# Optimization experiments

Hardware: AMD Instinct MI355X
Metric: run time of the kernel (lower is better)

## Reference

```python
import jax, jax.numpy as jnp
import numpy as np

D = 128          # hidden_channels
NU = 50000       # num user nodes
NI = 50000       # num item nodes
E = 600000       # edges per edge type
SLOPE = 0.01     # F.leaky_relu default negative_slope


def setup_inputs() -> dict:
    key = jax.random.key(0)
    ks = jax.random.split(key, 24)
    ws = 1.0 / np.sqrt(D)  # xavier-ish scale

    def W2(i):  # stacked [n_layers=2, D, D] weight
        return jax.random.normal(ks[i], (2, D, D), jnp.float32) * ws

    def B2(i):  # stacked [2, D] bias
        return jax.random.normal(ks[i], (2, D), jnp.float32) * 0.01

    inp = {
        "x_user": jax.random.normal(ks[0], (NU, D), jnp.float32),
        "x_item": jax.random.normal(ks[1], (NI, D), jnp.float32),
        # row 0 = src indices, row 1 = dst indices
        "ei_ui": jax.random.randint(ks[2], (2, E), 0, NU),  # user -> item (dst in [0,NI))
        "ei_iu": jax.random.randint(ks[3], (2, E), 0, NI),  # item -> user (dst in [0,NU))
        # per-node-type q/k/v Linear params, stacked over the 2 layers
        "q_w_user": W2(4),  "q_b_user": B2(5),
        "k_w_user": W2(6),  "k_b_user": B2(7),
        "v_w_user": W2(8),  "v_b_user": B2(9),
        "q_w_item": W2(10), "q_b_item": B2(11),
        "k_w_item": W2(12), "k_b_item": B2(13),
        "v_w_item": W2(14), "v_b_item": B2(15),
        # per-edge-type bilinear W, stacked over the 2 layers
        "W_ui": W2(16),
        "W_iu": W2(17),
    }
    return inp


def _edge_agg(x_src, x_dst, qw, qb, kw, kb, vw, vb, W, src, dst, n_dst):
    # torch Linear: x @ w.T + b
    q = x_src @ qw.T + qb            # [Nsrc, D]
    k = x_dst @ kw.T + kb            # [Ndst, D]
    v = x_src @ vw.T + vb            # [Nsrc, D]
    qW = q @ W                       # project on nodes (cheaper than per-edge)
    # per-edge bilinear score q_src . W . k_dst / sqrt(D)
    score = jnp.sum(qW[src] * k[dst], axis=-1) * (1.0 / np.sqrt(D))  # [E]
    alpha = jax.nn.softmax(jax.nn.leaky_relu(score, SLOPE))          # softmax over edges
    msg = alpha[:, None] * v[src]                                    # [E, D]
    return jax.ops.segment_sum(msg, dst, num_segments=n_dst)


def _layer(x_u, x_i, ei_ui, ei_iu, p, l):
    # edge type (user, rates, item): q/v from src type (user), k from dst type (item)
    agg_i = _edge_agg(x_u, x_i,
                      p["q_w_user"][l], p["q_b_user"][l],
                      p["k_w_item"][l], p["k_b_item"][l],
                      p["v_w_user"][l], p["v_b_user"][l],
                      p["W_ui"][l], ei_ui[0], ei_ui[1], NI)
    # edge type (item, rev_rates, user)
    agg_u = _edge_agg(x_i, x_u,
                      p["q_w_item"][l], p["q_b_item"][l],
                      p["k_w_user"][l], p["k_b_user"][l],
                      p["v_w_item"][l], p["v_b_item"][l],
                      p["W_iu"][l], ei_iu[0], ei_iu[1], NU)
    # out_dict initialized with x_dst.clone(), then scatter_add
    return x_u + agg_u, x_i + agg_i


def reference(x_user, x_item, ei_ui, ei_iu,
              q_w_user, q_b_user, k_w_user, k_b_user, v_w_user, v_b_user,
              q_w_item, q_b_item, k_w_item, k_b_item, v_w_item, v_b_item,
              W_ui, W_iu):
    p = dict(q_w_user=q_w_user, q_b_user=q_b_user, k_w_user=k_w_user,
             k_b_user=k_b_user, v_w_user=v_w_user, v_b_user=v_b_user,
             q_w_item=q_w_item, q_b_item=q_b_item, k_w_item=k_w_item,
             k_b_item=k_b_item, v_w_item=v_w_item, v_b_item=v_b_item,
             W_ui=W_ui, W_iu=W_iu)
    x_u, x_i = _layer(x_user, x_item, ei_ui, ei_iu, p, 0)  # conv1
    x_u, x_i = _layer(x_u, x_i, ei_ui, ei_iu, p, 1)        # conv2
    return jnp.concatenate([x_u, x_i], axis=0)  # [NU+NI, D]
```

## Files before the change

### kernel.cpp

```cpp
#include <hip/hip_runtime.h>
#include <stdint.h>

#define D 128

typedef __attribute__((ext_vector_type(8))) short bf16x8;
typedef __attribute__((ext_vector_type(4))) float f32x4;
typedef __attribute__((ext_vector_type(2))) float f32x2;
typedef unsigned short u16;
typedef unsigned char u8;
typedef unsigned int u32;

#define KSCALE (0.08838834764831845f * 1.4426950408889634f)

static __device__ __forceinline__ float b2f(u16 u) {
  return __uint_as_float(((unsigned)u) << 16);
}
static __device__ __forceinline__ u16 f2b(float f) {
  unsigned u = __float_as_uint(f);
  return (u16)((u + 0x7fffu + ((u >> 16) & 1u)) >> 16);
}

#if defined(__has_builtin)
#if __has_builtin(__builtin_amdgcn_cvt_pk_f32_fp8) && __has_builtin(__builtin_amdgcn_cvt_pk_fp8_f32)
#define HW_FP8 1
#endif
#endif

static __device__ __forceinline__ u8 enc_fp8(float f) {
#ifdef HW_FP8
  int p = __builtin_amdgcn_cvt_pk_fp8_f32(f, 0.f, 0, false);
  return (u8)(p & 0xff);
#else
  float a = fabsf(f);
  unsigned s = (__float_as_uint(f) >> 31) << 7;
  if (a < 7.8125e-3f) {
    int m = (int)(a * 512.f + 0.5f);
    if (m > 7) m = 7;
    return (u8)(s | m);
  }
  int e; float mant = frexpf(a, &e);
  int E = e + 6;
  int m = (int)((2.f * mant - 1.f) * 8.f + 0.5f);
  if (m == 8) { m = 0; E++; }
  if (E > 15 || (E == 15 && m > 6)) { E = 15; m = 6; }
  if (E < 1) return (u8)s;
  return (u8)(s | (E << 3) | m);
#endif
}

static __device__ __forceinline__ float dec1_fp8(u8 b) {
  int e = (b >> 3) & 15, m = b & 7;
  float mag = e ? ldexpf((float)(8 + m), e - 10) : ldexpf((float)m, -9);
  return (b & 128) ? -mag : mag;
}

static __device__ __forceinline__ void dec8_fp8(u32 lo, u32 hi, float* o) {
#ifdef HW_FP8
  f32x2 a = __builtin_amdgcn_cvt_pk_f32_fp8((int)lo, false);
  f32x2 b = __builtin_amdgcn_cvt_pk_f32_fp8((int)lo, true);
  f32x2 c = __builtin_amdgcn_cvt_pk_f32_fp8((int)hi, false);
  f32x2 d = __builtin_amdgcn_cvt_pk_f32_fp8((int)hi, true);
  o[0] = a.x; o[1] = a.y; o[2] = b.x; o[3] = b.y;
  o[4] = c.x; o[5] = c.y; o[6] = d.x; o[7] = d.y;
#else
  u32 w[2] = {lo, hi};
  u8* p = (u8*)w;
#pragma unroll
  for (int i = 0; i < 8; ++i) o[i] = dec1_fp8(p[i]);
#endif
}

template <int CTRL>
static __device__ __forceinline__ float dpp_add_f(float x) {
  int y = __builtin_amdgcn_update_dpp(0, __float_as_int(x), CTRL, 0xf, 0xf, true);
  return x + __int_as_float(y);
}

__global__ void prep_fused(const float* __restrict__ qwu, const float* __restrict__ qbu,
                           const float* __restrict__ qwi, const float* __restrict__ qbi,
                           const float* __restrict__ Wui, const float* __restrict__ Wiu,
                           u16* __restrict__ Mt, float* __restrict__ bq) {
  int c = blockIdx.y, d = blockIdx.x, j = threadIdx.x;
  int l = c & 1, type = c >> 1;
  const float* qw = (type ? qwi : qwu) + l * D * D;
  const float* qb = (type ? qbi : qbu) + l * D;
  const float* W  = (type ? Wiu : Wui) + l * D * D;
  float acc = 0.f;
  for (int cc = 0; cc < D; ++cc) acc += qw[cc * D + d] * W[cc * D + j];
  Mt[((size_t)c * D + j) * D + d] = f2b(acc);
  if (d == 0) {
    float ba = 0.f;
    for (int cc = 0; cc < D; ++cc) ba += qb[cc] * W[cc * D + j];
    bq[c * D + j] = ba;
  }
}

__global__ void cast_w(const float* __restrict__ kwu, const float* __restrict__ kwi,
                       const float* __restrict__ vwu, const float* __restrict__ vwi,
                       u16* __restrict__ Wb) {
  int y = blockIdx.y;
  const float* s = (y == 0) ? kwu : (y == 1) ? kwi : (y == 2) ? vwu : vwi;
  int i = blockIdx.x * 256 + threadIdx.x;
  Wb[(size_t)y * 2 * D * D + i] = f2b(s[i]);
}

__global__ void cast_x(const float* __restrict__ x, u16* __restrict__ xb, int n2) {
  int i = blockIdx.x * 256 + threadIdx.x;
  if (i < n2) {
    float2 v = ((const float2*)x)[i];
    ((unsigned*)xb)[i] = (unsigned)f2b(v.x) | ((unsigned)f2b(v.y) << 16);
  }
}

__global__ void zero_i(int* __restrict__ p, int n) {
  int i = blockIdx.x * 256 + threadIdx.x;
  if (i < n) p[i] = 0;
}

__global__ __launch_bounds__(256) void bhist(const int* __restrict__ dui,
                                             const int* __restrict__ diu,
                                             int* __restrict__ cnt_ui,
                                             int* __restrict__ cnt_iu, int E) {
  __shared__ int h[256];
  int t = threadIdx.x;
  h[t] = 0;
  __syncthreads();
  const int* dp = blockIdx.y ? diu : dui;
  int e0 = blockIdx.x * 1024;
#pragma unroll
  for (int i = 0; i < 4; ++i) {
    int e = e0 + i * 256 + t;
    if (e < E) atomicAdd(&h[dp[e] >> 8], 1);
  }
  __syncthreads();
  int* out = blockIdx.y ? cnt_iu : cnt_ui;
  if (h[t]) atomicAdd(&out[t], h[t]);
}

__global__ __launch_bounds__(256) void bscan(const int* __restrict__ cnt_ui,
                                             const int* __restrict__ cnt_iu,
                                             int* __restrict__ base_ui, int* __restrict__ base_iu,
                                             int* __restrict__ cur_ui, int* __restrict__ cur_iu,
                                             int* __restrict__ rp_ui, int* __restrict__ rp_iu,
                                             int nb_ui, int nb_iu, int n_ui, int n_iu, int E) {
  __shared__ int sh[256];
  int t = threadIdx.x;
  int v = (t < nb_ui) ? cnt_ui[t] : 0;
  sh[t] = v;
  __syncthreads();
  for (int off = 1; off < 256; off <<= 1) {
    int u = (t >= off) ? sh[t - off] : 0;
    __syncthreads();
    sh[t] += u;
    __syncthreads();
  }
  int ex = sh[t] - v;
  if (t < nb_ui) { base_ui[t] = ex; cur_ui[t] = ex; }
  if (t == 0) { base_ui[nb_ui] = E; rp_ui[n_ui] = E; }
  __syncthreads();
  v = (t < nb_iu) ? cnt_iu[t] : 0;
  sh[t] = v;
  __syncthreads();
  for (int off = 1; off < 256; off <<= 1) {
    int u = (t >= off) ? sh[t - off] : 0;
    __syncthreads();
    sh[t] += u;
    __syncthreads();
  }
  ex = sh[t] - v;
  if (t < nb_iu) { base_iu[t] = ex; cur_iu[t] = ex; }
  if (t == 0) { base_iu[nb_iu] = E; rp_iu[n_iu] = E; }
}

__global__ __launch_bounds__(256) void bscatter(
    const int* __restrict__ sui, const int* __restrict__ dui,
    const int* __restrict__ siu, const int* __restrict__ diu,
    int* __restrict__ cur_ui, int* __restrict__ cur_iu,
    u32* __restrict__ bb_ui, u32* __restrict__ bb_iu, int E) {
  __shared__ int h[256], rbase[256], c2[256];
  int t = threadIdx.x;
  const int* sp = blockIdx.y ? siu : sui;
  const int* dp = blockIdx.y ? diu : dui;
  int* gc = blockIdx.y ? cur_iu : cur_ui;
  u32* bb = blockIdx.y ? bb_iu : bb_ui;
  h[t] = 0;
  c2[t] = 0;
  __syncthreads();
  int e0 = blockIdx.x * 1024;
  u32 pr[4];
  int bk[4];
  bool act[4];
#pragma unroll
  for (int i = 0; i < 4; ++i) {
    int e = e0 + i * 256 + t;
    act[i] = e < E;
    if (act[i]) {
      int s = sp[e], d2 = dp[e];
      pr[i] = ((u32)d2 << 16) | (u32)s;
      bk[i] = d2 >> 8;
      atomicAdd(&h[bk[i]], 1);
    }
  }
  __syncthreads();
  if (h[t]) rbase[t] = atomicAdd(&gc[t], h[t]);
  __syncthreads();
#pragma unroll
  for (int i = 0; i < 4; ++i) {
    if (act[i]) {
      int r = atomicAdd(&c2[bk[i]], 1);
      bb[rbase[bk[i]] + r] = pr[i];
    }
  }
}

__global__ __launch_bounds__(256) void bsort(
    const u32* __restrict__ bb_ui, const u32* __restrict__ bb_iu,
    const int* __restrict__ base_ui, const int* __restrict__ base_iu,
    int* __restrict__ rp_ui, int* __restrict__ rp_iu,
    int* __restrict__ cs_ui, int* __restrict__ cs_iu,
    int nb_ui, int n_ui, int n_iu) {
  int b = blockIdx.x;
  const u32* bb; const int* base; int* rp; int* cs; int n;
  if (b < nb_ui) { bb = bb_ui; base = base_ui; rp = rp_ui; cs = cs_ui; n = n_ui; }
  else { b -= nb_ui; bb = bb_iu; base = base_iu; rp = rp_iu; cs = cs_iu; n = n_iu; }
  int lo = base[b], hi = base[b + 1];
  __shared__ int h[256], sh[256], cur[256];
  int t = threadIdx.x;
  h[t] = 0;
  __syncthreads();
  for (int j = lo + t; j < hi; j += 256) atomicAdd(&h[(bb[j] >> 16) & 255], 1);
  __syncthreads();
  int v = h[t];
  sh[t] = v;
  __syncthreads();
  for (int off = 1; off < 256; off <<= 1) {
    int u = (t >= off) ? sh[t - off] : 0;
    __syncthreads();
    sh[t] += u;
    __syncthreads();
  }
  int ex = lo + sh[t] - v;
  int gd = (b << 8) + t;
  if (gd < n) rp[gd] = ex;
  cur[t] = ex;
  __syncthreads();
  for (int j = lo + t; j < hi; j += 256) {
    u32 pr = bb[j];
    int p = atomicAdd(&cur[(pr >> 16) & 255], 1);
    cs[p] = (int)(pr & 0xffffu);
  }
}

__global__ __launch_bounds__(256) void gemm3(
    const u16* __restrict__ xu, const u16* __restrict__ xi,
    const u16* __restrict__ wqu, const u16* __restrict__ wku, const u16* __restrict__ wvu,
    const float* __restrict__ bqu, const float* __restrict__ bku, const float* __restrict__ bvu,
    const u16* __restrict__ wqi, const u16* __restrict__ wki, const u16* __restrict__ wvi,
    const float* __restrict__ bqi, const float* __restrict__ bki, const float* __restrict__ bvi,
    u8* __restrict__ Tqv_u, u16* __restrict__ Tk_u,
    u8* __restrict__ Tqv_i, u16* __restrict__ Tk_i,
    int gu, int nu, int ni) {
  __shared__ __align__(16) u16 wlds[128 * 136];
  int bx = blockIdx.x, y = blockIdx.y;
  bool item = bx >= gu;
  if (item) bx -= gu;
  const u16* x = item ? xi : xu;
  int nrows = item ? ni : nu;
  const u16* wt; const float* bias;
  if (y == 0)      { wt = item ? wqi : wqu; bias = item ? bqi : bqu; }
  else if (y == 1) { wt = item ? wki : wku; bias = item ? bki : bku; }
  else             { wt = item ? wvi : wvu; bias = item ? bvi : bvu; }
  u8* Tqv = item ? Tqv_i : Tqv_u;
  u16* Tk = item ? Tk_i : Tk_u;

  int t = threadIdx.x;
#pragma unroll
  for (int i = 0; i < 8; ++i) {
    int idx = t + 256 * i;
    int n = idx >> 4, kc = idx & 15;
    ((bf16x8*)wlds)[n * 17 + kc] = ((const bf16x8*)wt)[idx];
  }
  __syncthreads();
  int wave = t >> 6, lane = t & 63;
  int m = lane & 15, quad = lane >> 4;
  int row0 = bx * 64 + wave * 16;
  int arow = row0 + m;
  const bf16x8* xv = (const bf16x8*)(x + (size_t)(arow < nrows ? arow : 0) * D);
  f32x4 acc[8];
#pragma unroll
  for (int n = 0; n < 8; ++n) acc[n] = (f32x4){0.f, 0.f, 0.f, 0.f};
#pragma unroll
  for (int kk = 0; kk < 4; ++kk) {
    bf16x8 a = xv[kk * 4 + quad];
#pragma unroll
    for (int n = 0; n < 8; ++n) {
      bf16x8 b = ((const bf16x8*)wlds)[(n * 16 + m) * 17 + kk * 4 + quad];
      acc[n] = __builtin_amdgcn_mfma_f32_16x16x32_bf16(a, b, acc[n], 0, 0, 0);
    }
  }
  if (y == 1) {
#pragma unroll
    for (int n = 0; n < 8; ++n) {
      float bb = bias[n * 16 + m];
#pragma unroll
      for (int r = 0; r < 4; ++r) {
        int orow = row0 + quad * 4 + r;
        if (orow < nrows) Tk[(size_t)orow * D + n * 16 + m] = f2b((acc[n][r] + bb) * KSCALE);
      }
    }
  } else {
    int vo = (y == 0) ? 0 : 8;
#pragma unroll
    for (int n = 0; n < 8; ++n) {
      float bb = bias[n * 16 + m];
      int dim = n * 16 + m;
      int boff = ((dim >> 3) << 4) + (dim & 7) + vo;
#pragma unroll
      for (int r = 0; r < 4; ++r) {
        int orow = row0 + quad * 4 + r;
        if (orow < nrows) Tqv[(size_t)orow * 256 + boff] = enc_fp8(acc[n][r] + bb);
      }
    }
  }
}

static __device__ __forceinline__ void do_edge(uint4 w, bool act, const float* kx,
                                               float* acc, float& z) {
  float qx[8], vx[8];
  dec8_fp8(w.x, w.y, qx);
  dec8_fp8(w.z, w.w, vx);
  float dot = 0.f;
#pragma unroll
  for (int i = 0; i < 8; ++i) dot = fmaf(qx[i], kx[i], dot);
  dot = dpp_add_f<0xB1>(dot);
  dot = dpp_add_f<0x4E>(dot);
  dot = dpp_add_f<0x128>(dot);
  dot = dpp_add_f<0x124>(dot);
  float sc = (dot > 0.f) ? dot : 0.01f * dot;
  float p = act ? exp2f(sc) : 0.f;
  z += p;
#pragma unroll
  for (int i = 0; i < 8; ++i) acc[i] = fmaf(p, vx[i], acc[i]);
}

__global__ __launch_bounds__(256, 8) void agg_pass(
    const u8* __restrict__ Tqv_u, const u16* __restrict__ Tk_u,
    const u8* __restrict__ Tqv_i, const u16* __restrict__ Tk_i,
    const int* __restrict__ rp_ui, const int* __restrict__ cs_ui,
    const int* __restrict__ rp_iu, const int* __restrict__ cs_iu,
    float* __restrict__ agg_u, float* __restrict__ agg_i,
    float* __restrict__ zpart, int gai, int ni, int nu) {
  int bx = blockIdx.x;
  const u8* Pqv; const u16* Pk; const int* rp; const int* cs;
  float* agg; float* zp; int ndst;
  if (bx < gai) { Pqv = Tqv_u; Pk = Tk_i; rp = rp_ui; cs = cs_ui; agg = agg_i; zp = zpart; ndst = ni; }
  else { bx -= gai; Pqv = Tqv_i; Pk = Tk_u; rp = rp_iu; cs = cs_iu; agg = agg_u; zp = zpart + 1024; ndst = nu; }
  int wave = threadIdx.x >> 6, lane = threadIdx.x & 63;
  int d = bx * 4 + wave;
  int sub = lane & 15;
  int quad = lane >> 4;
  float z = 0.f;
  float acc[8] = {0.f, 0.f, 0.f, 0.f, 0.f, 0.f, 0.f, 0.f};
  if (d < ndst) {
    bf16x8 kf = *(const bf16x8*)(Pk + (size_t)d * D + sub * 8);
    int beg = rp[d], end = rp[d + 1];
    float kx[8];
#pragma unroll
    for (int i = 0; i < 8; ++i) kx[i] = b2f((u16)((short*)&kf)[i]);
    const u8* Pq = Pqv + sub * 16;
    for (int j = beg; j < end; j += 16) {
      int rem = end - j;
      int e1 = end - 1;
      int i0 = j + quad, i1 = i0 + 4, i2 = i0 + 8, i3 = i0 + 12;
      int s0 = cs[i0 < end ? i0 : e1];
      int s1 = cs[i1 < end ? i1 : e1];
      int s2 = cs[i2 < end ? i2 : e1];
      int s3 = cs[i3 < end ? i3 : e1];
      uint4 w0 = *(const uint4*)(Pq + (size_t)s0 * 256);
      uint4 w1 = *(const uint4*)(Pq + (size_t)s1 * 256);
      uint4 w2 = *(const uint4*)(Pq + (size_t)s2 * 256);
      uint4 w3 = *(const uint4*)(Pq + (size_t)s3 * 256);
      do_edge(w0, i0 < end, kx, acc, z);
      if (rem > 4)  do_edge(w1, i1 < end, kx, acc, z);
      if (rem > 8)  do_edge(w2, i2 < end, kx, acc, z);
      if (rem > 12) do_edge(w3, i3 < end, kx, acc, z);
    }
#pragma unroll
    for (int i = 0; i < 8; ++i) {
      acc[i] += __shfl_xor(acc[i], 16, 64);
      acc[i] += __shfl_xor(acc[i], 32, 64);
    }
    if (quad == 0) {
      float* ap = agg + (size_t)d * D + sub * 8;
      __builtin_nontemporal_store((f32x4){acc[0], acc[1], acc[2], acc[3]}, (f32x4*)ap);
      __builtin_nontemporal_store((f32x4){acc[4], acc[5], acc[6], acc[7]}, (f32x4*)ap + 1);
    }
    z += __shfl_xor(z, 16, 64);
    z += __shfl_xor(z, 32, 64);
  }
  __shared__ float ps[4];
  if (lane == 0) ps[wave] = z;
  __syncthreads();
  if (threadIdx.x == 0)
    unsafeAtomicAdd(&zp[blockIdx.x & 1023], ps[0] + ps[1] + ps[2] + ps[3]);
}

__global__ void zreduce(const float* __restrict__ zpart, float* __restrict__ zinv) {
  const float* zp = zpart + blockIdx.x * 1024;
  int t = threadIdx.x;
  float s = 0.f;
  for (int i = t; i < 1024; i += 256) s += zp[i];
  __shared__ float red[256];
  red[t] = s;
  __syncthreads();
  for (int k = 128; k > 0; k >>= 1) {
    if (t < k) red[t] += red[t + k];
    __syncthreads();
  }
  if (t == 0) zinv[blockIdx.x] = 1.0f / red[0];
}

__global__ void update_x(const float* __restrict__ xu, const float* __restrict__ xi,
                         const float* __restrict__ aggu, const float* __restrict__ aggi,
                         const float* __restrict__ zinv,
                         float* __restrict__ ou, float* __restrict__ oi,
                         u16* __restrict__ bu, u16* __restrict__ bi,
                         int nu, int ni, int wb) {
  int i = blockIdx.x * 256 + threadIdx.x;
  float zu = zinv[1];
  float zi = zinv[0];
  if (i < nu) {
    float v = xu[i] + aggu[i] * zu;
    ou[i] = v;
    if (wb) bu[i] = f2b(v);
  } else if (i < nu + ni) {
    int j = i - nu;
    float v = xi[j] + aggi[j] * zi;
    oi[j] = v;
    if (wb) bi[j] = f2b(v);
  }
}

extern "C" void kernel_launch(void* const* d_in, const int* in_sizes, int n_in,
                              void* d_out, int out_size, void* d_ws, size_t ws_size,
                              hipStream_t stream) {
  const float* xu_in = (const float*)d_in[0];
  const float* xi_in = (const float*)d_in[1];
  const int* ei_ui = (const int*)d_in[2];
  const int* ei_iu = (const int*)d_in[3];
  const float* qwu = (const float*)d_in[4];
  const float* qbu = (const float*)d_in[5];
  const float* kwu = (const float*)d_in[6];
  const float* kbu = (const float*)d_in[7];
  const float* vwu = (const float*)d_in[8];
  const float* vbu = (const float*)d_in[9];
  const float* qwi = (const float*)d_in[10];
  const float* qbi = (const float*)d_in[11];
  const float* kwi = (const float*)d_in[12];
  const float* kbi = (const float*)d_in[13];
  const float* vwi = (const float*)d_in[14];
  const float* vbi = (const float*)d_in[15];
  const float* Wui = (const float*)d_in[16];
  const float* Wiu = (const float*)d_in[17];

  int NU = in_sizes[0] / D;
  int NI = in_sizes[1] / D;
  int E  = in_sizes[2] / 2;

  char* w = (char*)d_ws;
  float* agg_u = (float*)w;  w += (size_t)NU * D * 4;
  float* agg_i = (float*)w;  w += (size_t)NI * D * 4;
  int* bcnt_ui = (int*)w;    w += 256 * 4;
  int* bcnt_iu = (int*)w;    w += 256 * 4;
  float* zpart = (float*)w;  w += 4096 * 4;
  float* zinv  = (float*)w;  w += 64;
  float* bq    = (float*)w;  w += 4 * D * 4;
  int* base_ui = (int*)w;    w += 260 * 4;
  int* base_iu = (int*)w;    w += 260 * 4;
  int* cur_ui  = (int*)w;    w += 256 * 4;
  int* cur_iu  = (int*)w;    w += 256 * 4;
  int* rp_ui = (int*)w;      w += (size_t)(NI + 4) * 4;
  int* rp_iu = (int*)w;      w += (size_t)(NU + 4) * 4;
  int* cs_ui = (int*)w;      w += (size_t)E * 4;
  int* cs_iu = (int*)w;      w += (size_t)E * 4;
  u32* bb_ui = (u32*)w;      w += (size_t)E * 4;
  u32* bb_iu = (u32*)w;      w += (size_t)E * 4;
  u16* Mt  = (u16*)w;        w += (size_t)4 * D * D * 2;
  u16* Wb  = (u16*)w;        w += (size_t)8 * D * D * 2;
  u16* xub = (u16*)w;        w += (size_t)NU * D * 2;
  u16* xib = (u16*)w;        w += (size_t)NI * D * 2;
  u16* Tk_u = (u16*)w;       w += (size_t)NU * D * 2;
  u16* Tk_i = (u16*)w;       w += (size_t)NI * D * 2;
  u8* Tqv_u = (u8*)w;        w += (size_t)NU * 256;
  u8* Tqv_i = (u8*)w;

  float* out_u = (float*)d_out;
  float* out_i = out_u + (size_t)NU * D;

  prep_fused<<<dim3(128, 4), 128, 0, stream>>>(qwu, qbu, qwi, qbi, Wui, Wiu, Mt, bq);
  cast_w<<<dim3(128, 4), 256, 0, stream>>>(kwu, kwi, vwu, vwi, Wb);
  cast_x<<<(NU * D / 2 + 255) / 256, 256, 0, stream>>>(xu_in, xub, NU * D / 2);
  cast_x<<<(NI * D / 2 + 255) / 256, 256, 0, stream>>>(xi_in, xib, NI * D / 2);

  int nb_ui = (NI + 255) >> 8;
  int nb_iu = (NU + 255) >> 8;
  zero_i<<<18, 256, 0, stream>>>(bcnt_ui, 512 + 4096);
  int geb = (E + 1023) / 1024;
  bhist<<<dim3(geb, 2), 256, 0, stream>>>(ei_ui + E, ei_iu + E, bcnt_ui, bcnt_iu, E);
  bscan<<<1, 256, 0, stream>>>(bcnt_ui, bcnt_iu, base_ui, base_iu, cur_ui, cur_iu,
                               rp_ui, rp_iu, nb_ui, nb_iu, NI, NU, E);
  bscatter<<<dim3(geb, 2), 256, 0, stream>>>(ei_ui, ei_ui + E, ei_iu, ei_iu + E,
                                             cur_ui, cur_iu, bb_ui, bb_iu, E);
  bsort<<<nb_ui + nb_iu, 256, 0, stream>>>(bb_ui, bb_iu, base_ui, base_iu,
                                           rp_ui, rp_iu, cs_ui, cs_iu, nb_ui, NI, NU);

  int gu = (NU + 63) / 64, gi = (NI + 63) / 64;
  int gau = (NU + 3) / 4, gai = (NI + 3) / 4;
  int gup = (NU * D + NI * D + 255) / 256;

  for (int l = 0; l < 2; ++l) {
    gemm3<<<dim3(gu + gi, 3), 256, 0, stream>>>(
        xub, xib,
        Mt + (size_t)l * D * D, Wb + (size_t)(0 + l) * D * D, Wb + (size_t)(4 + l) * D * D,
        bq + l * D, kbu + l * D, vbu + l * D,
        Mt + (size_t)(2 + l) * D * D, Wb + (size_t)(2 + l) * D * D, Wb + (size_t)(6 + l) * D * D,
        bq + (2 + l) * D, kbi + l * D, vbi + l * D,
        Tqv_u, Tk_u, Tqv_i, Tk_i, gu, NU, NI);
    agg_pass<<<gai + gau, 256, 0, stream>>>(
        Tqv_u, Tk_u, Tqv_i, Tk_i, rp_ui, cs_ui, rp_iu, cs_iu,
        agg_u, agg_i, zpart + (size_t)l * 2 * 1024, gai, NI, NU);
    zreduce<<<2, 256, 0, stream>>>(zpart + (size_t)l * 2 * 1024, zinv + l * 2);
    if (l == 0)
      update_x<<<gup, 256, 0, stream>>>(xu_in, xi_in, agg_u, agg_i, zinv + l * 2,
                                        out_u, out_i, xub, xib, NU * D, NI * D, 1);
    else
      update_x<<<gup, 256, 0, stream>>>(out_u, out_i, agg_u, agg_i, zinv + l * 2,
                                        out_u, out_i, nullptr, nullptr, NU * D, NI * D, 0);
  }
}
```

Baseline: 489.7 us.

## Store q and k in fp16 with split q/v tables, use fdot2 for edge scores

Q and K projections are now written as fp16 and V stays fp8. The interleaved q/v fp8 table is split into a separate fp16 Q table and an fp8 V table. Edge scoring uses packed fp16 dot2 instructions in place of decoding fp8 and bf16 to float. This removes conversion ALU work and improves score accuracy, but the per-edge gathered bytes grow from 16 to 24 across two separate random loads. update_x is also vectorised to float4 accesses.

```diff
diff --git a/kernel.cpp b/kernel.cpp
--- a/kernel.cpp
+++ b/kernel.cpp
@@ -6,6 +6,7 @@
 typedef __attribute__((ext_vector_type(8))) short bf16x8;
 typedef __attribute__((ext_vector_type(4))) float f32x4;
 typedef __attribute__((ext_vector_type(2))) float f32x2;
+typedef __attribute__((ext_vector_type(2))) _Float16 h2;
 typedef unsigned short u16;
 typedef unsigned char u8;
 typedef unsigned int u32;
@@ -19,10 +20,17 @@
   unsigned u = __float_as_uint(f);
   return (u16)((u + 0x7fffu + ((u >> 16) & 1u)) >> 16);
 }
+static __device__ __forceinline__ u16 f2h(float f) {
+  _Float16 h = (_Float16)f;
+  return __builtin_bit_cast(unsigned short, h);
+}
 
 #if defined(__has_builtin)
 #if __has_builtin(__builtin_amdgcn_cvt_pk_f32_fp8) && __has_builtin(__builtin_amdgcn_cvt_pk_fp8_f32)
 #define HW_FP8 1
+#endif
+#if __has_builtin(__builtin_amdgcn_fdot2)
+#define HW_DOT2 1
 #endif
 #endif
 
@@ -257,8 +265,8 @@
     const float* __restrict__ bqu, const float* __restrict__ bku, const float* __restrict__ bvu,
     const u16* __restrict__ wqi, const u16* __restrict__ wki, const u16* __restrict__ wvi,
     const float* __restrict__ bqi, const float* __restrict__ bki, const float* __restrict__ bvi,
-    u8* __restrict__ Tqv_u, u16* __restrict__ Tk_u,
-    u8* __restrict__ Tqv_i, u16* __restrict__ Tk_i,
+    u16* __restrict__ Tq_u, u16* __restrict__ Tk_u, u8* __restrict__ Tv_u,
+    u16* __restrict__ Tq_i, u16* __restrict__ Tk_i, u8* __restrict__ Tv_i,
     int gu, int nu, int ni) {
   __shared__ __align__(16) u16 wlds[128 * 136];
   int bx = blockIdx.x, y = blockIdx.y;
@@ -270,8 +278,9 @@
   if (y == 0)      { wt = item ? wqi : wqu; bias = item ? bqi : bqu; }
   else if (y == 1) { wt = item ? wki : wku; bias = item ? bki : bku; }
   else             { wt = item ? wvi : wvu; bias = item ? bvi : bvu; }
-  u8* Tqv = item ? Tqv_i : Tqv_u;
+  u16* Tq = item ? Tq_i : Tq_u;
   u16* Tk = item ? Tk_i : Tk_u;
+  u8*  Tv = item ? Tv_i : Tv_u;
 
   int t = threadIdx.x;
 #pragma unroll
@@ -298,40 +307,61 @@
       acc[n] = __builtin_amdgcn_mfma_f32_16x16x32_bf16(a, b, acc[n], 0, 0, 0);
     }
   }
-  if (y == 1) {
-#pragma unroll
-    for (int n = 0; n < 8; ++n) {
-      float bb = bias[n * 16 + m];
-#pragma unroll
-      for (int r = 0; r < 4; ++r) {
-        int orow = row0 + quad * 4 + r;
-        if (orow < nrows) Tk[(size_t)orow * D + n * 16 + m] = f2b((acc[n][r] + bb) * KSCALE);
-      }
-    }
-  } else {
-    int vo = (y == 0) ? 0 : 8;
+  if (y == 0) {
 #pragma unroll
     for (int n = 0; n < 8; ++n) {
       float bb = bias[n * 16 + m];
       int dim = n * 16 + m;
-      int boff = ((dim >> 3) << 4) + (dim & 7) + vo;
 #pragma unroll
       for (int r = 0; r < 4; ++r) {
         int orow = row0 + quad * 4 + r;
-        if (orow < nrows) Tqv[(size_t)orow * 256 + boff] = enc_fp8(acc[n][r] + bb);
+        if (orow < nrows) Tq[(size_t)orow * D + dim] = f2h(acc[n][r] + bb);
       }
     }
-  }
-}
-
-static __device__ __forceinline__ void do_edge(uint4 w, bool act, const float* kx,
-                                               float* acc, float& z) {
-  float qx[8], vx[8];
-  dec8_fp8(w.x, w.y, qx);
-  dec8_fp8(w.z, w.w, vx);
-  float dot = 0.f;
-#pragma unroll
-  for (int i = 0; i < 8; ++i) dot = fmaf(qx[i], kx[i], dot);
+  } else if (y == 1) {
+#pragma unroll
+    for (int n = 0; n < 8; ++n) {
+      float bb = bias[n * 16 + m];
+      int dim = n * 16 + m;
+#pragma unroll
+      for (int r = 0; r < 4; ++r) {
+        int orow = row0 + quad * 4 + r;
+        if (orow < nrows) Tk[(size_t)orow * D + dim] = f2h((acc[n][r] + bb) * KSCALE);
+      }
+    }
+  } else {
+#pragma unroll
+    for (int n = 0; n < 8; ++n) {
+      float bb = bias[n * 16 + m];
+      int dim = n * 16 + m;
+#pragma unroll
+      for (int r = 0; r < 4; ++r) {
+        int orow = row0 + quad * 4 + r;
+        if (orow < nrows) Tv[(size_t)orow * D + dim] = enc_fp8(acc[n][r] + bb);
+      }
+    }
+  }
+}
+
+static __device__ __forceinline__ void do_edge(uint4 qw, uint2 vw, bool act,
+                                               const u32* kp, float* acc, float& z) {
+  float dot;
+#ifdef HW_DOT2
+  dot = __builtin_amdgcn_fdot2(__builtin_bit_cast(h2, qw.x), __builtin_bit_cast(h2, kp[0]), 0.f, false);
+  dot = __builtin_amdgcn_fdot2(__builtin_bit_cast(h2, qw.y), __builtin_bit_cast(h2, kp[1]), dot, false);
+  dot = __builtin_amdgcn_fdot2(__builtin_bit_cast(h2, qw.z), __builtin_bit_cast(h2, kp[2]), dot, false);
+  dot = __builtin_amdgcn_fdot2(__builtin_bit_cast(h2, qw.w), __builtin_bit_cast(h2, kp[3]), dot, false);
+#else
+  dot = 0.f;
+  u32 qa[4] = {qw.x, qw.y, qw.z, qw.w};
+#pragma unroll
+  for (int i = 0; i < 4; ++i) {
+    h2 qh = __builtin_bit_cast(h2, qa[i]);
+    h2 kh = __builtin_bit_cast(h2, kp[i]);
+    dot = fmaf((float)qh.x, (float)kh.x, dot);
+    dot = fmaf((float)qh.y, (float)kh.y, dot);
+  }
+#endif
   dot = dpp_add_f<0xB1>(dot);
   dot = dpp_add_f<0x4E>(dot);
   dot = dpp_add_f<0x128>(dot);
@@ -339,22 +369,24 @@
   float sc = (dot > 0.f) ? dot : 0.01f * dot;
   float p = act ? exp2f(sc) : 0.f;
   z += p;
+  float vx[8];
+  dec8_fp8(vw.x, vw.y, vx);
 #pragma unroll
   for (int i = 0; i < 8; ++i) acc[i] = fmaf(p, vx[i], acc[i]);
 }
 
 __global__ __launch_bounds__(256, 8) void agg_pass(
-    const u8* __restrict__ Tqv_u, const u16* __restrict__ Tk_u,
-    const u8* __restrict__ Tqv_i, const u16* __restrict__ Tk_i,
+    const u16* __restrict__ Tq_u, const u16* __restrict__ Tk_u, const u8* __restrict__ Tv_u,
+    const u16* __restrict__ Tq_i, const u16* __restrict__ Tk_i, const u8* __restrict__ Tv_i,
     const int* __restrict__ rp_ui, const int* __restrict__ cs_ui,
     const int* __restrict__ rp_iu, const int* __restrict__ cs_iu,
     float* __restrict__ agg_u, float* __restrict__ agg_i,
     float* __restrict__ zpart, int gai, int ni, int nu) {
   int bx = blockIdx.x;
-  const u8* Pqv; const u16* Pk; const int* rp; const int* cs;
+  const u16* Pq; const u16* Pk; const u8* Pv; const int* rp; const int* cs;
   float* agg; float* zp; int ndst;
-  if (bx < gai) { Pqv = Tqv_u; Pk = Tk_i; rp = rp_ui; cs = cs_ui; agg = agg_i; zp = zpart; ndst = ni; }
-  else { bx -= gai; Pqv = Tqv_i; Pk = Tk_u; rp = rp_iu; cs = cs_iu; agg = agg_u; zp = zpart + 1024; ndst = nu; }
+  if (bx < gai) { Pq = Tq_u; Pk = Tk_i; Pv = Tv_u; rp = rp_ui; cs = cs_ui; agg = agg_i; zp = zpart; ndst = ni; }
+  else { bx -= gai; Pq = Tq_i; Pk = Tk_u; Pv = Tv_i; rp = rp_iu; cs = cs_iu; agg = agg_u; zp = zpart + 1024; ndst = nu; }
   int wave = threadIdx.x >> 6, lane = threadIdx.x & 63;
   int d = bx * 4 + wave;
   int sub = lane & 15;
@@ -362,12 +394,11 @@
   float z = 0.f;
   float acc[8] = {0.f, 0.f, 0.f, 0.f, 0.f, 0.f, 0.f, 0.f};
   if (d < ndst) {
-    bf16x8 kf = *(const bf16x8*)(Pk + (size_t)d * D + sub * 8);
+    uint4 kf = *(const uint4*)(Pk + (size_t)d * D + sub * 8);
+    u32 kp[4] = {kf.x, kf.y, kf.z, kf.w};
     int beg = rp[d], end = rp[d + 1];
-    float kx[8];
-#pragma unroll
-    for (int i = 0; i < 8; ++i) kx[i] = b2f((u16)((short*)&kf)[i]);
-    const u8* Pq = Pqv + sub * 16;
+    const u16* Pqs = Pq + sub * 8;
+    const u8* Pvs = Pv + sub * 8;
     for (int j = beg; j < end; j += 16) {
       int rem = end - j;
       int e1 = end - 1;
@@ -376,14 +407,18 @@
       int s1 = cs[i1 < end ? i1 : e1];
       int s2 = cs[i2 < end ? i2 : e1];
       int s3 = cs[i3 < end ? i3 : e1];
-      uint4 w0 = *(const uint4*)(Pq + (size_t)s0 * 256);
-      uint4 w1 = *(const uint4*)(Pq + (size_t)s1 * 256);
-      uint4 w2 = *(const uint4*)(Pq + (size_t)s2 * 256);
-      uint4 w3 = *(const uint4*)(Pq + (size_t)s3 * 256);
-      do_edge(w0, i0 < end, kx, acc, z);
-      if (rem > 4)  do_edge(w1, i1 < end, kx, acc, z);
-      if (rem > 8)  do_edge(w2, i2 < end, kx, acc, z);
-      if (rem > 12) do_edge(w3, i3 < end, kx, acc, z);
+      uint4 q0 = *(const uint4*)(Pqs + (size_t)s0 * D);
+      uint4 q1 = *(const uint4*)(Pqs + (size_t)s1 * D);
+      uint4 q2 = *(const uint4*)(Pqs + (size_t)s2 * D);
+      uint4 q3 = *(const uint4*)(Pqs + (size_t)s3 * D);
+      uint2 v0 = *(const uint2*)(Pvs + (size_t)s0 * D);
+      uint2 v1 = *(const uint2*)(Pvs + (size_t)s1 * D);
+      uint2 v2 = *(const uint2*)(Pvs + (size_t)s2 * D);
+      uint2 v3 = *(const uint2*)(Pvs + (size_t)s3 * D);
+      do_edge(q0, v0, i0 < end, kp, acc, z);
+      if (rem > 4)  do_edge(q1, v1, i1 < end, kp, acc, z);
+      if (rem > 8)  do_edge(q2, v2, i2 < end, kp, acc, z);
+      if (rem > 12) do_edge(q3, v3, i3 < end, kp, acc, z);
     }
 #pragma unroll
     for (int i = 0; i < 8; ++i) {
@@ -425,19 +460,33 @@
                          const float* __restrict__ zinv,
                          float* __restrict__ ou, float* __restrict__ oi,
                          u16* __restrict__ bu, u16* __restrict__ bi,
-                         int nu, int ni, int wb) {
+                         int nu4, int ni4, int wb) {
   int i = blockIdx.x * 256 + threadIdx.x;
   float zu = zinv[1];
   float zi = zinv[0];
-  if (i < nu) {
-    float v = xu[i] + aggu[i] * zu;
-    ou[i] = v;
-    if (wb) bu[i] = f2b(v);
-  } else if (i < nu + ni) {
-    int j = i - nu;
-    float v = xi[j] + aggi[j] * zi;
-    oi[j] = v;
-    if (wb) bi[j] = f2b(v);
+  const float4* xs; const float4* as; float4* os; u16* bs; float zz; int jj;
+  if (i < nu4) {
+    xs = (const float4*)xu; as = (const float4*)aggu; os = (float4*)ou; bs = bu;
+    zz = zu; jj = i;
+  } else if (i < nu4 + ni4) {
+    jj = i - nu4;
+    xs = (const float4*)xi; as = (const float4*)aggi; os = (float4*)oi; bs = bi;
+    zz = zi;
+  } else {
+    return;
+  }
+  float4 xv = xs[jj];
+  float4 av = as[jj];
+  float4 v;
+  v.x = xv.x + av.x * zz;
+  v.y = xv.y + av.y * zz;
+  v.z = xv.z + av.z * zz;
+  v.w = xv.w + av.w * zz;
+  os[jj] = v;
+  if (wb) {
+    ushort4 b;
+    b.x = f2b(v.x); b.y = f2b(v.y); b.z = f2b(v.z); b.w = f2b(v.w);
+    ((ushort4*)bs)[jj] = b;
   }
 }
 
@@ -491,8 +540,10 @@
   u16* xib = (u16*)w;        w += (size_t)NI * D * 2;
   u16* Tk_u = (u16*)w;       w += (size_t)NU * D * 2;
   u16* Tk_i = (u16*)w;       w += (size_t)NI * D * 2;
-  u8* Tqv_u = (u8*)w;        w += (size_t)NU * 256;
-  u8* Tqv_i = (u8*)w;
+  u16* Tq_u = (u16*)w;       w += (size_t)NU * D * 2;
+  u16* Tq_i = (u16*)w;       w += (size_t)NI * D * 2;
+  u8* Tv_u = (u8*)w;         w += (size_t)NU * D;
+  u8* Tv_i = (u8*)w;
 
   float* out_u = (float*)d_out;
   float* out_i = out_u + (size_t)NU * D;
@@ -516,7 +567,8 @@
 
   int gu = (NU + 63) / 64, gi = (NI + 63) / 64;
   int gau = (NU + 3) / 4, gai = (NI + 3) / 4;
-  int gup = (NU * D + NI * D + 255) / 256;
+  int nu4 = NU * D / 4, ni4 = NI * D / 4;
+  int gup = (nu4 + ni4 + 255) / 256;
 
   for (int l = 0; l < 2; ++l) {
     gemm3<<<dim3(gu + gi, 3), 256, 0, stream>>>(
@@ -525,16 +577,16 @@
         bq + l * D, kbu + l * D, vbu + l * D,
         Mt + (size_t)(2 + l) * D * D, Wb + (size_t)(2 + l) * D * D, Wb + (size_t)(6 + l) * D * D,
         bq + (2 + l) * D, kbi + l * D, vbi + l * D,
-        Tqv_u, Tk_u, Tqv_i, Tk_i, gu, NU, NI);
+        Tq_u, Tk_u, Tv_u, Tq_i, Tk_i, Tv_i, gu, NU, NI);
     agg_pass<<<gai + gau, 256, 0, stream>>>(
-        Tqv_u, Tk_u, Tqv_i, Tk_i, rp_ui, cs_ui, rp_iu, cs_iu,
+        Tq_u, Tk_u, Tv_u, Tq_i, Tk_i, Tv_i, rp_ui, cs_ui, rp_iu, cs_iu,
         agg_u, agg_i, zpart + (size_t)l * 2 * 1024, gai, NI, NU);
     zreduce<<<2, 256, 0, stream>>>(zpart + (size_t)l * 2 * 1024, zinv + l * 2);
     if (l == 0)
       update_x<<<gup, 256, 0, stream>>>(xu_in, xi_in, agg_u, agg_i, zinv + l * 2,
-                                        out_u, out_i, xub, xib, NU * D, NI * D, 1);
+                                        out_u, out_i, xub, xib, nu4, ni4, 1);
     else
       update_x<<<gup, 256, 0, stream>>>(out_u, out_i, agg_u, agg_i, zinv + l * 2,
-                                        out_u, out_i, nullptr, nullptr, NU * D, NI * D, 0);
-  }
-}
+                                        out_u, out_i, nullptr, nullptr, nu4, ni4, 0);
+  }
+}
```

Measured after the change: 483.4 us. No clear change (-1.3%).
